# Optimization experiments

Measured on AMD Instinct MI355X. Metric: run time of the kernel, lower is better.

Reference implementation:

```python
import jax, jax.numpy as jnp
import numpy as np

B, D, M, H, L = 65536, 512, 128, 4, 2  # batch, token_dim, model_dim, heads, layers
HD = M // H
EPS = 1e-5


def _ln(x, g, b):
    m = jnp.mean(x, axis=-1, keepdims=True)
    v = jnp.mean((x - m) ** 2, axis=-1, keepdims=True)
    return (x - m) / jnp.sqrt(v + EPS) * g + b


def _mha(q, k, wqkv, bqkv, wo, bo):
    # q, k: [B, 1, M]; torch MultiheadAttention with packed in_proj ([3M, M])
    qp = jnp.einsum('bsm,nm->bsn', q, wqkv[:M]) + bqkv[:M]
    kp = jnp.einsum('bsm,nm->bsn', k, wqkv[M:2 * M]) + bqkv[M:2 * M]
    vp = jnp.einsum('bsm,nm->bsn', k, wqkv[2 * M:]) + bqkv[2 * M:]
    qh = qp.reshape(qp.shape[0], -1, H, HD).transpose(0, 2, 1, 3)
    kh = kp.reshape(kp.shape[0], -1, H, HD).transpose(0, 2, 1, 3)
    vh = vp.reshape(vp.shape[0], -1, H, HD).transpose(0, 2, 1, 3)
    scores = jnp.einsum('bhqd,bhkd->bhqk', qh, kh) / float(np.sqrt(HD))
    attn = jax.nn.softmax(scores, axis=-1)  # kv_len == 1 -> weights are 1
    o = jnp.einsum('bhqk,bhkd->bhqd', attn, vh).transpose(0, 2, 1, 3).reshape(qp.shape)
    return jnp.einsum('bsm,nm->bsn', o, wo) + bo


def _ffn(x, w1, b1, w2, b2):
    h = jax.nn.relu(jnp.einsum('bsm,nm->bsn', x, w1) + b1)
    return jnp.einsum('bsn,mn->bsm', h, w2) + b2


def _forward(transformer_tokens, eda_proj_w, eda_proj_b, imu_proj_w, imu_proj_b,
             eda_cls, imu_cls, e2i_wqkv, e2i_bqkv, e2i_wo, e2i_bo,
             i2e_wqkv, i2e_bqkv, i2e_wo, i2e_bo,
             ffn_eda_w1, ffn_eda_b1, ffn_eda_w2, ffn_eda_b2,
             ffn_imu_w1, ffn_imu_b1, ffn_imu_w2, ffn_imu_b2,
             ln_eda1_g, ln_eda1_b, ln_eda2_g, ln_eda2_b,
             ln_imu1_g, ln_imu1_b, ln_imu2_g, ln_imu2_b,
             out_w, out_b, out_ln_g, out_ln_b):
    eda_raw = transformer_tokens[:, 0, :]
    imu_raw = transformer_tokens[:, 1, :]
    eda = (jnp.einsum('bd,md->bm', eda_raw, eda_proj_w) + eda_proj_b)[:, None, :] + eda_cls
    imu = (jnp.einsum('bd,md->bm', imu_raw, imu_proj_w) + imu_proj_b)[:, None, :] + imu_cls
    for l in range(L):
        eda_attn = _mha(eda, imu, e2i_wqkv[l], e2i_bqkv[l], e2i_wo[l], e2i_bo[l])
        eda = _ln(eda + eda_attn, ln_eda1_g[l], ln_eda1_b[l])
        eda = _ln(eda + _ffn(eda, ffn_eda_w1[l], ffn_eda_b1[l], ffn_eda_w2[l], ffn_eda_b2[l]),
                  ln_eda2_g[l], ln_eda2_b[l])
        imu_attn = _mha(imu, eda, i2e_wqkv[l], i2e_bqkv[l], i2e_wo[l], i2e_bo[l])
        imu = _ln(imu + imu_attn, ln_imu1_g[l], ln_imu1_b[l])
        imu = _ln(imu + _ffn(imu, ffn_imu_w1[l], ffn_imu_b1[l], ffn_imu_w2[l], ffn_imu_b2[l]),
                  ln_imu2_g[l], ln_imu2_b[l])
    fused = jnp.concatenate([eda[:, 0, :], imu[:, 0, :]], axis=-1)  # [B, 2M]
    out = jnp.einsum('bn,mn->bm', fused, out_w) + out_b
    return jax.nn.relu(_ln(out, out_ln_g, out_ln_b))  # [B, M]


def setup_inputs() -> dict:
    key = jax.random.key(0)
    ks = jax.random.split(key, 16)
    n = lambda k, s: jax.random.normal(k, s, dtype=jnp.float32) * 0.02
    return dict(
        transformer_tokens=jax.random.normal(ks[0], (B, 2, D), dtype=jnp.float32),
        eda_proj_w=n(ks[1], (M, D)), eda_proj_b=jnp.zeros((M,), jnp.float32),
        imu_proj_w=n(ks[2], (M, D)), imu_proj_b=jnp.zeros((M,), jnp.float32),
        eda_cls=jnp.zeros((1, 1, M), jnp.float32), imu_cls=jnp.zeros((1, 1, M), jnp.float32),
        e2i_wqkv=n(ks[3], (L, 3 * M, M)), e2i_bqkv=jnp.zeros((L, 3 * M), jnp.float32),
        e2i_wo=n(ks[4], (L, M, M)), e2i_bo=jnp.zeros((L, M), jnp.float32),
        i2e_wqkv=n(ks[5], (L, 3 * M, M)), i2e_bqkv=jnp.zeros((L, 3 * M), jnp.float32),
        i2e_wo=n(ks[6], (L, M, M)), i2e_bo=jnp.zeros((L, M), jnp.float32),
        ffn_eda_w1=n(ks[7], (L, 2 * M, M)), ffn_eda_b1=jnp.zeros((L, 2 * M), jnp.float32),
        ffn_eda_w2=n(ks[8], (L, M, 2 * M)), ffn_eda_b2=jnp.zeros((L, M), jnp.float32),
        ffn_imu_w1=n(ks[9], (L, 2 * M, M)), ffn_imu_b1=jnp.zeros((L, 2 * M), jnp.float32),
        ffn_imu_w2=n(ks[10], (L, M, 2 * M)), ffn_imu_b2=jnp.zeros((L, M), jnp.float32),
        ln_eda1_g=jnp.ones((L, M), jnp.float32), ln_eda1_b=jnp.zeros((L, M), jnp.float32),
        ln_eda2_g=jnp.ones((L, M), jnp.float32), ln_eda2_b=jnp.zeros((L, M), jnp.float32),
        ln_imu1_g=jnp.ones((L, M), jnp.float32), ln_imu1_b=jnp.zeros((L, M), jnp.float32),
        ln_imu2_g=jnp.ones((L, M), jnp.float32), ln_imu2_b=jnp.zeros((L, M), jnp.float32),
        out_w=n(ks[11], (M, 2 * M)), out_b=jnp.zeros((M,), jnp.float32),
        out_ln_g=jnp.ones((M,), jnp.float32), out_ln_b=jnp.zeros((M,), jnp.float32),
    )


def reference(transformer_tokens, eda_proj_w, eda_proj_b, imu_proj_w, imu_proj_b,
              eda_cls, imu_cls, e2i_wqkv, e2i_bqkv, e2i_wo, e2i_bo,
              i2e_wqkv, i2e_bqkv, i2e_wo, i2e_bo,
              ffn_eda_w1, ffn_eda_b1, ffn_eda_w2, ffn_eda_b2,
              ffn_imu_w1, ffn_imu_b1, ffn_imu_w2, ffn_imu_b2,
              ln_eda1_g, ln_eda1_b, ln_eda2_g, ln_eda2_b,
              ln_imu1_g, ln_imu1_b, ln_imu2_g, ln_imu2_b,
              out_w, out_b, out_ln_g, out_ln_b):
    return _forward(transformer_tokens, eda_proj_w, eda_proj_b, imu_proj_w, imu_proj_b,
                    eda_cls, imu_cls, e2i_wqkv, e2i_bqkv, e2i_wo, e2i_bo,
                    i2e_wqkv, i2e_bqkv, i2e_wo, i2e_bo,
                    ffn_eda_w1, ffn_eda_b1, ffn_eda_w2, ffn_eda_b2,
                    ffn_imu_w1, ffn_imu_b1, ffn_imu_w2, ffn_imu_b2,
                    ln_eda1_g, ln_eda1_b, ln_eda2_g, ln_eda2_b,
                    ln_imu1_g, ln_imu1_b, ln_imu2_g, ln_imu2_b,
                    out_w, out_b, out_ln_g, out_ln_b)
```

## Files before the change

kernel.cpp:

```cpp
#include <hip/hip_runtime.h>
#include <hip/hip_bf16.h>


typedef __bf16 bf16x8_t __attribute__((ext_vector_type(8)));
typedef float  f32x16_t __attribute__((ext_vector_type(16)));
typedef float  f32x4_t  __attribute__((ext_vector_type(4)));

#define DEV static __device__ __forceinline__

DEV f32x16_t mfma_op(bf16x8_t a, bf16x8_t b, f32x16_t c) {
  return __builtin_amdgcn_mfma_f32_32x32x16_bf16(a, b, c, 0, 0, 0);
}

DEV bf16x8_t cvt8(const float* p) {
  f32x4_t t0 = *(const f32x4_t*)p;
  f32x4_t t1 = *(const f32x4_t*)(p + 4);
  bf16x8_t a;
  a[0] = (__bf16)t0[0]; a[1] = (__bf16)t0[1]; a[2] = (__bf16)t0[2]; a[3] = (__bf16)t0[3];
  a[4] = (__bf16)t1[0]; a[5] = (__bf16)t1[1]; a[6] = (__bf16)t1[2]; a[7] = (__bf16)t1[3];
  return a;
}

constexpr int PO_PROJ_E = 0;
constexpr int PO_PROJ_I = PO_PROJ_E + 128 * 512;
constexpr int PO_ATTN   = PO_PROJ_I + 128 * 512;
constexpr int PO_FFN1   = PO_ATTN   + 4 * 32 * 512;
constexpr int PO_FFN2   = PO_FFN1   + 4 * 64 * 512;
constexpr int PO_HEAD   = PO_FFN2   + 4 * 64 * 512;
constexpr int WS_BC_F      = 4 * 128 * 128;
constexpr int WS_PACK_BYTE = (WS_BC_F + 4 * 128) * 4;

#define PITCH_S 136
#define PITCH_H 40

__global__ __launch_bounds__(64) void prep_combine(
    const float* __restrict__ e2i_wqkv, const float* __restrict__ e2i_wo,
    const float* __restrict__ e2i_bqkv, const float* __restrict__ e2i_bo,
    const float* __restrict__ i2e_wqkv, const float* __restrict__ i2e_wo,
    const float* __restrict__ i2e_bqkv, const float* __restrict__ i2e_bo,
    float* __restrict__ wsf) {
  const int blk = blockIdx.x;
  const int d = blk >> 7, n = blk & 127, l = d & 1;
  const float* wqkv = (d < 2) ? e2i_wqkv : i2e_wqkv;
  const float* wo   = (d < 2) ? e2i_wo   : i2e_wo;
  const float* bqkv = (d < 2) ? e2i_bqkv : i2e_bqkv;
  const float* bo   = (d < 2) ? e2i_bo   : i2e_bo;
  const float* wv    = wqkv + l * 3 * 128 * 128 + 2 * 128 * 128;
  const float* worow = wo + l * 128 * 128 + n * 128;
  const float* bv    = bqkv + l * 3 * 128 + 2 * 128;
  const int lane = threadIdx.x;
  float a0 = 0.f, a1 = 0.f;
  for (int p = 0; p < 128; ++p) {
    float w = worow[p];
    a0 += w * wv[p * 128 + lane];
    a1 += w * wv[p * 128 + 64 + lane];
  }
  wsf[d * 16384 + n * 128 + lane]      = a0;
  wsf[d * 16384 + n * 128 + 64 + lane] = a1;
  float bacc = worow[lane] * bv[lane] + worow[64 + lane] * bv[64 + lane];
  for (int off = 1; off < 64; off <<= 1) bacc += __shfl_xor(bacc, off, 64);
  if (lane == 0) wsf[WS_BC_F + d * 128 + n] = bacc + bo[l * 128 + n];
}

__global__ __launch_bounds__(64) void prep_pack(
    const float* __restrict__ proj_e, const float* __restrict__ proj_i,
    const float* __restrict__ ffn_e_w1, const float* __restrict__ ffn_i_w1,
    const float* __restrict__ ffn_e_w2, const float* __restrict__ ffn_i_w2,
    const float* __restrict__ out_w, const float* __restrict__ wsf,
    __bf16* __restrict__ pack) {
  const int b = blockIdx.x, lane = threadIdx.x;
  const float* src; int K, sh, dstOff, c;
  if (b < 128)      { src = proj_e; K = 512; sh = 2; dstOff = PO_PROJ_E; c = b; }
  else if (b < 256) { src = proj_i; K = 512; sh = 2; dstOff = PO_PROJ_I; c = b - 128; }
  else if (b < 384) { int i = (b - 256) >> 5; c = (b - 256) & 31;
                      src = wsf + i * 16384; K = 128; sh = 2;
                      dstOff = PO_ATTN + i * 32 * 512; }
  else if (b < 640) { int i = (b - 384) >> 6; c = (b - 384) & 63;
                      src = ((i < 2) ? ffn_e_w1 : ffn_i_w1) + (i & 1) * 256 * 128;
                      K = 128; sh = 3; dstOff = PO_FFN1 + i * 64 * 512; }
  else if (b < 896) { int i = (b - 640) >> 6; c = (b - 640) & 63;
                      src = ((i < 2) ? ffn_e_w2 : ffn_i_w2) + (i & 1) * 128 * 256;
                      K = 256; sh = 2; dstOff = PO_FFN2 + i * 64 * 512; }
  else              { c = b - 896; src = out_w; K = 256; sh = 2; dstOff = PO_HEAD; }
  const int kt = c >> sh, nt = c & ((1 << sh) - 1);
  const int n  = nt * 32 + (lane & 31);
  const int kb = kt * 16 + (lane >> 5) * 8;
  const float* s = src + n * K + kb;
  bf16x8_t v;
#pragma unroll
  for (int j = 0; j < 8; ++j) v[j] = (__bf16)s[j];
  *(bf16x8_t*)&pack[dstOff + (c * 64 + lane) * 8] = v;
}

__global__ __launch_bounds__(64, 2) void fused_fwd(
    const float* __restrict__ tokens,
    const float* __restrict__ eda_proj_b, const float* __restrict__ eda_cls,
    const float* __restrict__ imu_proj_b, const float* __restrict__ imu_cls,
    const float* __restrict__ ffn_eda_b1, const float* __restrict__ ffn_eda_b2,
    const float* __restrict__ ffn_imu_b1, const float* __restrict__ ffn_imu_b2,
    const float* __restrict__ ln_e1g, const float* __restrict__ ln_e1b,
    const float* __restrict__ ln_e2g, const float* __restrict__ ln_e2b,
    const float* __restrict__ ln_i1g, const float* __restrict__ ln_i1b,
    const float* __restrict__ ln_i2g, const float* __restrict__ ln_i2b,
    const float* __restrict__ out_b, const float* __restrict__ out_ln_g,
    const float* __restrict__ out_ln_b,
    const float* __restrict__ bc_all,
    const __bf16* __restrict__ pack,
    float* __restrict__ out) {
  alignas(16) __shared__ __bf16 smem[2 * 32 * PITCH_S + 32 * PITCH_H];
  __bf16* Se = smem;
  __bf16* Si = smem + 32 * PITCH_S;
  __bf16* Sh = smem + 2 * 32 * PITCH_S;

  const int lane = threadIdx.x;
  const int l31 = lane & 31, lh = lane >> 5;
  const int rowbase = blockIdx.x * 32;

  auto crowf = [&](int r) { return (r & 3) + ((r >> 2) << 3) + (lh << 2); };

  auto layer_norm = [&](f32x16_t (&A)[4], const float* g, const float* bb) {
    float gv[4], bv[4];
#pragma unroll
    for (int nt = 0; nt < 4; ++nt) { gv[nt] = g[nt * 32 + l31]; bv[nt] = bb[nt * 32 + l31]; }
#pragma unroll
    for (int r = 0; r < 16; ++r) {
      float s = 0.f, s2 = 0.f;
#pragma unroll
      for (int nt = 0; nt < 4; ++nt) { float v = A[nt][r]; s += v; s2 += v * v; }
#pragma unroll
      for (int off = 1; off < 32; off <<= 1) {
        s  += __shfl_xor(s, off, 64);
        s2 += __shfl_xor(s2, off, 64);
      }
      const float mean = s * (1.f / 128.f);
      const float var  = s2 * (1.f / 128.f) - mean * mean;
      const float rs   = rsqrtf(var + 1e-5f);
#pragma unroll
      for (int nt = 0; nt < 4; ++nt)
        A[nt][r] = (A[nt][r] - mean) * rs * gv[nt] + bv[nt];
    }
  };

  auto store_state = [&](f32x16_t (&A)[4], __bf16* S) {
#pragma unroll
    for (int nt = 0; nt < 4; ++nt)
#pragma unroll
      for (int r = 0; r < 16; ++r)
        S[crowf(r) * PITCH_S + nt * 32 + l31] = (__bf16)A[nt][r];
  };

#pragma unroll 1
  for (int sel = 0; sel < 2; ++sel) {
    const float* pb = sel ? imu_proj_b : eda_proj_b;
    const float* pc = sel ? imu_cls : eda_cls;
    __bf16* Sd = sel ? Si : Se;
    const __bf16* pw = pack + (sel ? PO_PROJ_I : PO_PROJ_E);
    f32x16_t acc[4];
#pragma unroll
    for (int nt = 0; nt < 4; ++nt) {
      const float bias = pb[nt * 32 + l31] + pc[nt * 32 + l31];
#pragma unroll
      for (int r = 0; r < 16; ++r) acc[nt][r] = bias;
    }
    const float* t0 = tokens + (size_t)(rowbase + l31) * 1024 + sel * 512 + lh * 8;
#pragma unroll 1
    for (int kt = 0; kt < 32; ++kt) {
      bf16x8_t a0 = cvt8(t0 + kt * 16);
      const __bf16* pwk = pw + (kt * 4 * 64 + lane) * 8;
#pragma unroll
      for (int nt = 0; nt < 4; ++nt)
        acc[nt] = mfma_op(a0, *(const bf16x8_t*)(pwk + nt * 512), acc[nt]);
    }
    store_state(acc, Sd);
  }

#pragma unroll 1
  for (int l = 0; l < 2; ++l) {
#pragma unroll 1
    for (int mod = 0; mod < 2; ++mod) {
      const __bf16* Sx = mod ? Se : Si;
      __bf16* St = mod ? Si : Se;
      const int widx = mod * 2 + l;
      const __bf16* attn_w = pack + PO_ATTN + widx * 32 * 512;
      const __bf16* ffn1_w = pack + PO_FFN1 + widx * 64 * 512;
      const __bf16* ffn2_w = pack + PO_FFN2 + widx * 64 * 512;
      const float* bc  = bc_all + widx * 128;
      const float* b1  = (mod ? ffn_imu_b1 : ffn_eda_b1) + l * 256;
      const float* b2  = (mod ? ffn_imu_b2 : ffn_eda_b2) + l * 128;
      const float* g1  = (mod ? ln_i1g : ln_e1g) + l * 128;
      const float* bb1 = (mod ? ln_i1b : ln_e1b) + l * 128;
      const float* g2  = (mod ? ln_i2g : ln_e2g) + l * 128;
      const float* bb2 = (mod ? ln_i2b : ln_e2b) + l * 128;

      f32x16_t acc[4];
#pragma unroll
      for (int nt = 0; nt < 4; ++nt) {
        const float bv = bc[nt * 32 + l31];
#pragma unroll
        for (int r = 0; r < 16; ++r)
          acc[nt][r] = bv + (float)St[crowf(r) * PITCH_S + nt * 32 + l31];
      }
#pragma unroll 1
      for (int kt = 0; kt < 8; ++kt) {
        bf16x8_t a0 = *(const bf16x8_t*)&Sx[l31 * PITCH_S + kt * 16 + lh * 8];
        const __bf16* wk = attn_w + (kt * 4 * 64 + lane) * 8;
#pragma unroll
        for (int nt = 0; nt < 4; ++nt)
          acc[nt] = mfma_op(a0, *(const bf16x8_t*)(wk + nt * 512), acc[nt]);
      }
      layer_norm(acc, g1, bb1);
      store_state(acc, St);

      f32x16_t yacc[4];
#pragma unroll
      for (int nt = 0; nt < 4; ++nt) {
        const float bv = b2[nt * 32 + l31];
#pragma unroll
        for (int r = 0; r < 16; ++r) yacc[nt][r] = bv + acc[nt][r];
      }
#pragma unroll 1
      for (int hc = 0; hc < 8; ++hc) {
        f32x16_t h;
        {
          const float hb = b1[hc * 32 + l31];
#pragma unroll
          for (int r = 0; r < 16; ++r) h[r] = hb;
        }
        const __bf16* w1k = ffn1_w + (hc * 64 + lane) * 8;
#pragma unroll
        for (int kt = 0; kt < 8; ++kt) {
          bf16x8_t a0 = *(const bf16x8_t*)&St[l31 * PITCH_S + kt * 16 + lh * 8];
          h = mfma_op(a0, *(const bf16x8_t*)(w1k + kt * 8 * 512), h);
        }
#pragma unroll
        for (int r = 0; r < 16; ++r)
          Sh[crowf(r) * PITCH_H + l31] = (__bf16)fmaxf(h[r], 0.f);
#pragma unroll
        for (int kt2 = 0; kt2 < 2; ++kt2) {
          bf16x8_t ah = *(const bf16x8_t*)&Sh[l31 * PITCH_H + kt2 * 16 + lh * 8];
          const __bf16* w2k = ffn2_w + (((hc * 2 + kt2) * 4) * 64 + lane) * 8;
#pragma unroll
          for (int nt = 0; nt < 4; ++nt)
            yacc[nt] = mfma_op(ah, *(const bf16x8_t*)(w2k + nt * 512), yacc[nt]);
        }
      }
      layer_norm(yacc, g2, bb2);
      store_state(yacc, St);
    }
  }

  {
    f32x16_t acc[4];
#pragma unroll
    for (int nt = 0; nt < 4; ++nt) {
      const float bv = out_b[nt * 32 + l31];
#pragma unroll
      for (int r = 0; r < 16; ++r) acc[nt][r] = bv;
    }
#pragma unroll 1
    for (int kt = 0; kt < 16; ++kt) {
      const __bf16* Sa = (kt < 8) ? Se : Si;
      const int ko = (kt & 7) * 16 + lh * 8;
      bf16x8_t a0 = *(const bf16x8_t*)&Sa[l31 * PITCH_S + ko];
      const __bf16* wk = pack + PO_HEAD + (kt * 4 * 64 + lane) * 8;
#pragma unroll
      for (int nt = 0; nt < 4; ++nt)
        acc[nt] = mfma_op(a0, *(const bf16x8_t*)(wk + nt * 512), acc[nt]);
    }
    layer_norm(acc, out_ln_g, out_ln_b);
#pragma unroll
    for (int nt = 0; nt < 4; ++nt)
#pragma unroll
      for (int r = 0; r < 16; ++r)
        out[(rowbase + crowf(r)) * 128 + nt * 32 + l31] = fmaxf(acc[nt][r], 0.f);
  }
}

extern "C" void kernel_launch(void* const* d_in, const int* in_sizes, int n_in,
                              void* d_out, int out_size, void* d_ws, size_t ws_size,
                              hipStream_t stream) {
  const float* tokens     = (const float*)d_in[0];
  const float* eda_proj_w = (const float*)d_in[1];
  const float* eda_proj_b = (const float*)d_in[2];
  const float* imu_proj_w = (const float*)d_in[3];
  const float* imu_proj_b = (const float*)d_in[4];
  const float* eda_cls    = (const float*)d_in[5];
  const float* imu_cls    = (const float*)d_in[6];
  const float* e2i_wqkv   = (const float*)d_in[7];
  const float* e2i_bqkv   = (const float*)d_in[8];
  const float* e2i_wo     = (const float*)d_in[9];
  const float* e2i_bo     = (const float*)d_in[10];
  const float* i2e_wqkv   = (const float*)d_in[11];
  const float* i2e_bqkv   = (const float*)d_in[12];
  const float* i2e_wo     = (const float*)d_in[13];
  const float* i2e_bo     = (const float*)d_in[14];
  const float* ffn_eda_w1 = (const float*)d_in[15];
  const float* ffn_eda_b1 = (const float*)d_in[16];
  const float* ffn_eda_w2 = (const float*)d_in[17];
  const float* ffn_eda_b2 = (const float*)d_in[18];
  const float* ffn_imu_w1 = (const float*)d_in[19];
  const float* ffn_imu_b1 = (const float*)d_in[20];
  const float* ffn_imu_w2 = (const float*)d_in[21];
  const float* ffn_imu_b2 = (const float*)d_in[22];
  const float* ln_eda1_g  = (const float*)d_in[23];
  const float* ln_eda1_b  = (const float*)d_in[24];
  const float* ln_eda2_g  = (const float*)d_in[25];
  const float* ln_eda2_b  = (const float*)d_in[26];
  const float* ln_imu1_g  = (const float*)d_in[27];
  const float* ln_imu1_b  = (const float*)d_in[28];
  const float* ln_imu2_g  = (const float*)d_in[29];
  const float* ln_imu2_b  = (const float*)d_in[30];
  const float* out_w      = (const float*)d_in[31];
  const float* out_b      = (const float*)d_in[32];
  const float* out_ln_g   = (const float*)d_in[33];
  const float* out_ln_b   = (const float*)d_in[34];

  float*  wsf  = (float*)d_ws;
  __bf16* pack = (__bf16*)((char*)d_ws + WS_PACK_BYTE);

  prep_combine<<<dim3(512), dim3(64), 0, stream>>>(
      e2i_wqkv, e2i_wo, e2i_bqkv, e2i_bo,
      i2e_wqkv, i2e_wo, i2e_bqkv, i2e_bo, wsf);

  prep_pack<<<dim3(960), dim3(64), 0, stream>>>(
      eda_proj_w, imu_proj_w, ffn_eda_w1, ffn_imu_w1,
      ffn_eda_w2, ffn_imu_w2, out_w, wsf, pack);

  fused_fwd<<<dim3(2048), dim3(64), 0, stream>>>(
      tokens, eda_proj_b, eda_cls, imu_proj_b, imu_cls,
      ffn_eda_b1, ffn_eda_b2, ffn_imu_b1, ffn_imu_b2,
      ln_eda1_g, ln_eda1_b, ln_eda2_g, ln_eda2_b,
      ln_imu1_g, ln_imu1_b, ln_imu2_g, ln_imu2_b,
      out_b, out_ln_g, out_ln_b,
      wsf + WS_BC_F, pack, (float*)d_out);
}
```

Measured before the change: 653.1 us.

## Software-pipeline MFMA operand loads and split prep_combine reduction across four waves

The GEMM loops in the fused forward kernel (input projection, attention, FFN, head) now use explicit double buffering: the next k-step's token and weight fragments are loaded while the current MFMAs run, and in the FFN all state and weight fragments for a hidden chunk are loaded up front. This is meant to hide global and LDS load latency in a kernel that runs one wave per block. prep_combine now uses 256 threads, splitting the 128-term dot product across four waves with an LDS reduction, which shortens the serial loop. The price is higher register pressure, which could cause spills or lower occupancy.

```diff
diff --git a/kernel.cpp b/kernel.cpp
--- a/kernel.cpp
+++ b/kernel.cpp
@@ -12,9 +12,7 @@
   return __builtin_amdgcn_mfma_f32_32x32x16_bf16(a, b, c, 0, 0, 0);
 }
 
-DEV bf16x8_t cvt8(const float* p) {
-  f32x4_t t0 = *(const f32x4_t*)p;
-  f32x4_t t1 = *(const f32x4_t*)(p + 4);
+DEV bf16x8_t cvt2(f32x4_t t0, f32x4_t t1) {
   bf16x8_t a;
   a[0] = (__bf16)t0[0]; a[1] = (__bf16)t0[1]; a[2] = (__bf16)t0[2]; a[3] = (__bf16)t0[3];
   a[4] = (__bf16)t1[0]; a[5] = (__bf16)t1[1]; a[6] = (__bf16)t1[2]; a[7] = (__bf16)t1[3];
@@ -33,7 +31,7 @@
 #define PITCH_S 136
 #define PITCH_H 40
 
-__global__ __launch_bounds__(64) void prep_combine(
+__global__ __launch_bounds__(256) void prep_combine(
     const float* __restrict__ e2i_wqkv, const float* __restrict__ e2i_wo,
     const float* __restrict__ e2i_bqkv, const float* __restrict__ e2i_bo,
     const float* __restrict__ i2e_wqkv, const float* __restrict__ i2e_wo,
@@ -48,18 +46,29 @@
   const float* wv    = wqkv + l * 3 * 128 * 128 + 2 * 128 * 128;
   const float* worow = wo + l * 128 * 128 + n * 128;
   const float* bv    = bqkv + l * 3 * 128 + 2 * 128;
-  const int lane = threadIdx.x;
-  float a0 = 0.f, a1 = 0.f;
-  for (int p = 0; p < 128; ++p) {
-    float w = worow[p];
-    a0 += w * wv[p * 128 + lane];
-    a1 += w * wv[p * 128 + 64 + lane];
+  const int tid = threadIdx.x, lane = tid & 63, w = tid >> 6;
+  float a0 = 0.f, a1 = 0.f, c0 = 0.f, c1 = 0.f;
+#pragma unroll 4
+  for (int p = w * 32; p < w * 32 + 32; p += 2) {
+    float wa = worow[p], wb = worow[p + 1];
+    a0 += wa * wv[p * 128 + lane];
+    a1 += wa * wv[p * 128 + 64 + lane];
+    c0 += wb * wv[(p + 1) * 128 + lane];
+    c1 += wb * wv[(p + 1) * 128 + 64 + lane];
   }
-  wsf[d * 16384 + n * 128 + lane]      = a0;
-  wsf[d * 16384 + n * 128 + 64 + lane] = a1;
-  float bacc = worow[lane] * bv[lane] + worow[64 + lane] * bv[64 + lane];
-  for (int off = 1; off < 64; off <<= 1) bacc += __shfl_xor(bacc, off, 64);
-  if (lane == 0) wsf[WS_BC_F + d * 128 + n] = bacc + bo[l * 128 + n];
+  a0 += c0; a1 += c1;
+  __shared__ float red[4][2][64];
+  red[w][0][lane] = a0; red[w][1][lane] = a1;
+  __syncthreads();
+  if (w == 0) {
+    a0 = red[0][0][lane] + red[1][0][lane] + red[2][0][lane] + red[3][0][lane];
+    a1 = red[0][1][lane] + red[1][1][lane] + red[2][1][lane] + red[3][1][lane];
+    wsf[d * 16384 + n * 128 + lane]      = a0;
+    wsf[d * 16384 + n * 128 + 64 + lane] = a1;
+    float bacc = worow[lane] * bv[lane] + worow[64 + lane] * bv[64 + lane];
+    for (int off = 1; off < 64; off <<= 1) bacc += __shfl_xor(bacc, off, 64);
+    if (lane == 0) wsf[WS_BC_F + d * 128 + n] = bacc + bo[l * 128 + n];
+  }
 }
 
 __global__ __launch_bounds__(64) void prep_pack(
@@ -163,13 +172,43 @@
       for (int r = 0; r < 16; ++r) acc[nt][r] = bias;
     }
     const float* t0 = tokens + (size_t)(rowbase + l31) * 1024 + sel * 512 + lh * 8;
-#pragma unroll 1
-    for (int kt = 0; kt < 32; ++kt) {
-      bf16x8_t a0 = cvt8(t0 + kt * 16);
-      const __bf16* pwk = pw + (kt * 4 * 64 + lane) * 8;
-#pragma unroll
-      for (int nt = 0; nt < 4; ++nt)
-        acc[nt] = mfma_op(a0, *(const bf16x8_t*)(pwk + nt * 512), acc[nt]);
+    f32x4_t tA0 = *(const f32x4_t*)t0, tA1 = *(const f32x4_t*)(t0 + 4);
+    const __bf16* pA = pw + lane * 8;
+    bf16x8_t wA0 = *(const bf16x8_t*)(pA);
+    bf16x8_t wA1 = *(const bf16x8_t*)(pA + 512);
+    bf16x8_t wA2 = *(const bf16x8_t*)(pA + 1024);
+    bf16x8_t wA3 = *(const bf16x8_t*)(pA + 1536);
+#pragma unroll 1
+    for (int kt = 0; kt < 32; kt += 2) {
+      const float* tb = t0 + (kt + 1) * 16;
+      f32x4_t tB0 = *(const f32x4_t*)tb, tB1 = *(const f32x4_t*)(tb + 4);
+      const __bf16* pB = pw + ((kt + 1) * 4 * 64 + lane) * 8;
+      bf16x8_t wB0 = *(const bf16x8_t*)(pB);
+      bf16x8_t wB1 = *(const bf16x8_t*)(pB + 512);
+      bf16x8_t wB2 = *(const bf16x8_t*)(pB + 1024);
+      bf16x8_t wB3 = *(const bf16x8_t*)(pB + 1536);
+      {
+        bf16x8_t a = cvt2(tA0, tA1);
+        acc[0] = mfma_op(a, wA0, acc[0]);
+        acc[1] = mfma_op(a, wA1, acc[1]);
+        acc[2] = mfma_op(a, wA2, acc[2]);
+        acc[3] = mfma_op(a, wA3, acc[3]);
+      }
+      const int ka = (kt + 2 < 32) ? kt + 2 : kt;
+      const float* ta = t0 + ka * 16;
+      tA0 = *(const f32x4_t*)ta; tA1 = *(const f32x4_t*)(ta + 4);
+      pA = pw + (ka * 4 * 64 + lane) * 8;
+      wA0 = *(const bf16x8_t*)(pA);
+      wA1 = *(const bf16x8_t*)(pA + 512);
+      wA2 = *(const bf16x8_t*)(pA + 1024);
+      wA3 = *(const bf16x8_t*)(pA + 1536);
+      {
+        bf16x8_t a = cvt2(tB0, tB1);
+        acc[0] = mfma_op(a, wB0, acc[0]);
+        acc[1] = mfma_op(a, wB1, acc[1]);
+        acc[2] = mfma_op(a, wB2, acc[2]);
+        acc[3] = mfma_op(a, wB3, acc[3]);
+      }
     }
     store_state(acc, Sd);
   }
@@ -200,13 +239,37 @@
         for (int r = 0; r < 16; ++r)
           acc[nt][r] = bv + (float)St[crowf(r) * PITCH_S + nt * 32 + l31];
       }
-#pragma unroll 1
-      for (int kt = 0; kt < 8; ++kt) {
-        bf16x8_t a0 = *(const bf16x8_t*)&Sx[l31 * PITCH_S + kt * 16 + lh * 8];
-        const __bf16* wk = attn_w + (kt * 4 * 64 + lane) * 8;
-#pragma unroll
-        for (int nt = 0; nt < 4; ++nt)
-          acc[nt] = mfma_op(a0, *(const bf16x8_t*)(wk + nt * 512), acc[nt]);
+      {
+        bf16x8_t aA = *(const bf16x8_t*)&Sx[l31 * PITCH_S + lh * 8];
+        const __bf16* pA = attn_w + lane * 8;
+        bf16x8_t wA0 = *(const bf16x8_t*)(pA);
+        bf16x8_t wA1 = *(const bf16x8_t*)(pA + 512);
+        bf16x8_t wA2 = *(const bf16x8_t*)(pA + 1024);
+        bf16x8_t wA3 = *(const bf16x8_t*)(pA + 1536);
+#pragma unroll 1
+        for (int kt = 0; kt < 8; kt += 2) {
+          bf16x8_t aB = *(const bf16x8_t*)&Sx[l31 * PITCH_S + (kt + 1) * 16 + lh * 8];
+          const __bf16* pB = attn_w + ((kt + 1) * 4 * 64 + lane) * 8;
+          bf16x8_t wB0 = *(const bf16x8_t*)(pB);
+          bf16x8_t wB1 = *(const bf16x8_t*)(pB + 512);
+          bf16x8_t wB2 = *(const bf16x8_t*)(pB + 1024);
+          bf16x8_t wB3 = *(const bf16x8_t*)(pB + 1536);
+          acc[0] = mfma_op(aA, wA0, acc[0]);
+          acc[1] = mfma_op(aA, wA1, acc[1]);
+          acc[2] = mfma_op(aA, wA2, acc[2]);
+          acc[3] = mfma_op(aA, wA3, acc[3]);
+          const int ka = (kt + 2 < 8) ? kt + 2 : kt;
+          aA = *(const bf16x8_t*)&Sx[l31 * PITCH_S + ka * 16 + lh * 8];
+          pA = attn_w + (ka * 4 * 64 + lane) * 8;
+          wA0 = *(const bf16x8_t*)(pA);
+          wA1 = *(const bf16x8_t*)(pA + 512);
+          wA2 = *(const bf16x8_t*)(pA + 1024);
+          wA3 = *(const bf16x8_t*)(pA + 1536);
+          acc[0] = mfma_op(aB, wB0, acc[0]);
+          acc[1] = mfma_op(aB, wB1, acc[1]);
+          acc[2] = mfma_op(aB, wB2, acc[2]);
+          acc[3] = mfma_op(aB, wB3, acc[3]);
+        }
       }
       layer_norm(acc, g1, bb1);
       store_state(acc, St);
@@ -220,29 +283,55 @@
       }
 #pragma unroll 1
       for (int hc = 0; hc < 8; ++hc) {
+        bf16x8_t s0 = *(const bf16x8_t*)&St[l31 * PITCH_S + 0 * 16 + lh * 8];
+        bf16x8_t s1 = *(const bf16x8_t*)&St[l31 * PITCH_S + 1 * 16 + lh * 8];
+        bf16x8_t s2 = *(const bf16x8_t*)&St[l31 * PITCH_S + 2 * 16 + lh * 8];
+        bf16x8_t s3 = *(const bf16x8_t*)&St[l31 * PITCH_S + 3 * 16 + lh * 8];
+        bf16x8_t s4 = *(const bf16x8_t*)&St[l31 * PITCH_S + 4 * 16 + lh * 8];
+        bf16x8_t s5 = *(const bf16x8_t*)&St[l31 * PITCH_S + 5 * 16 + lh * 8];
+        bf16x8_t s6 = *(const bf16x8_t*)&St[l31 * PITCH_S + 6 * 16 + lh * 8];
+        bf16x8_t s7 = *(const bf16x8_t*)&St[l31 * PITCH_S + 7 * 16 + lh * 8];
+        const __bf16* w1b = ffn1_w + (hc * 64 + lane) * 8;
+        bf16x8_t u0 = *(const bf16x8_t*)(w1b + 0 * 8 * 512);
+        bf16x8_t u1 = *(const bf16x8_t*)(w1b + 1 * 8 * 512);
+        bf16x8_t u2 = *(const bf16x8_t*)(w1b + 2 * 8 * 512);
+        bf16x8_t u3 = *(const bf16x8_t*)(w1b + 3 * 8 * 512);
+        bf16x8_t u4 = *(const bf16x8_t*)(w1b + 4 * 8 * 512);
+        bf16x8_t u5 = *(const bf16x8_t*)(w1b + 5 * 8 * 512);
+        bf16x8_t u6 = *(const bf16x8_t*)(w1b + 6 * 8 * 512);
+        bf16x8_t u7 = *(const bf16x8_t*)(w1b + 7 * 8 * 512);
+        const __bf16* w2b = ffn2_w + (hc * 8 * 64 + lane) * 8;
+        bf16x8_t v0 = *(const bf16x8_t*)(w2b + 0 * 512);
+        bf16x8_t v1 = *(const bf16x8_t*)(w2b + 1 * 512);
+        bf16x8_t v2 = *(const bf16x8_t*)(w2b + 2 * 512);
+        bf16x8_t v3 = *(const bf16x8_t*)(w2b + 3 * 512);
+        bf16x8_t v4 = *(const bf16x8_t*)(w2b + 4 * 512);
+        bf16x8_t v5 = *(const bf16x8_t*)(w2b + 5 * 512);
+        bf16x8_t v6 = *(const bf16x8_t*)(w2b + 6 * 512);
+        bf16x8_t v7 = *(const bf16x8_t*)(w2b + 7 * 512);
         f32x16_t h;
         {
           const float hb = b1[hc * 32 + l31];
 #pragma unroll
           for (int r = 0; r < 16; ++r) h[r] = hb;
         }
-        const __bf16* w1k = ffn1_w + (hc * 64 + lane) * 8;
-#pragma unroll
-        for (int kt = 0; kt < 8; ++kt) {
-          bf16x8_t a0 = *(const bf16x8_t*)&St[l31 * PITCH_S + kt * 16 + lh * 8];
-          h = mfma_op(a0, *(const bf16x8_t*)(w1k + kt * 8 * 512), h);
-        }
+        h = mfma_op(s0, u0, h); h = mfma_op(s1, u1, h);
+        h = mfma_op(s2, u2, h); h = mfma_op(s3, u3, h);
+        h = mfma_op(s4, u4, h); h = mfma_op(s5, u5, h);
+        h = mfma_op(s6, u6, h); h = mfma_op(s7, u7, h);
 #pragma unroll
         for (int r = 0; r < 16; ++r)
           Sh[crowf(r) * PITCH_H + l31] = (__bf16)fmaxf(h[r], 0.f);
-#pragma unroll
-        for (int kt2 = 0; kt2 < 2; ++kt2) {
-          bf16x8_t ah = *(const bf16x8_t*)&Sh[l31 * PITCH_H + kt2 * 16 + lh * 8];
-          const __bf16* w2k = ffn2_w + (((hc * 2 + kt2) * 4) * 64 + lane) * 8;
-#pragma unroll
-          for (int nt = 0; nt < 4; ++nt)
-            yacc[nt] = mfma_op(ah, *(const bf16x8_t*)(w2k + nt * 512), yacc[nt]);
-        }
+        bf16x8_t ah0 = *(const bf16x8_t*)&Sh[l31 * PITCH_H + lh * 8];
+        bf16x8_t ah1 = *(const bf16x8_t*)&Sh[l31 * PITCH_H + 16 + lh * 8];
+        yacc[0] = mfma_op(ah0, v0, yacc[0]);
+        yacc[1] = mfma_op(ah0, v1, yacc[1]);
+        yacc[2] = mfma_op(ah0, v2, yacc[2]);
+        yacc[3] = mfma_op(ah0, v3, yacc[3]);
+        yacc[0] = mfma_op(ah1, v4, yacc[0]);
+        yacc[1] = mfma_op(ah1, v5, yacc[1]);
+        yacc[2] = mfma_op(ah1, v6, yacc[2]);
+        yacc[3] = mfma_op(ah1, v7, yacc[3]);
       }
       layer_norm(yacc, g2, bb2);
       store_state(yacc, St);
@@ -257,15 +346,38 @@
 #pragma unroll
       for (int r = 0; r < 16; ++r) acc[nt][r] = bv;
     }
-#pragma unroll 1
-    for (int kt = 0; kt < 16; ++kt) {
-      const __bf16* Sa = (kt < 8) ? Se : Si;
-      const int ko = (kt & 7) * 16 + lh * 8;
-      bf16x8_t a0 = *(const bf16x8_t*)&Sa[l31 * PITCH_S + ko];
-      const __bf16* wk = pack + PO_HEAD + (kt * 4 * 64 + lane) * 8;
-#pragma unroll
-      for (int nt = 0; nt < 4; ++nt)
-        acc[nt] = mfma_op(a0, *(const bf16x8_t*)(wk + nt * 512), acc[nt]);
+    const __bf16* hw = pack + PO_HEAD;
+    bf16x8_t aA = *(const bf16x8_t*)&Se[l31 * PITCH_S + lh * 8];
+    const __bf16* pA = hw + lane * 8;
+    bf16x8_t wA0 = *(const bf16x8_t*)(pA);
+    bf16x8_t wA1 = *(const bf16x8_t*)(pA + 512);
+    bf16x8_t wA2 = *(const bf16x8_t*)(pA + 1024);
+    bf16x8_t wA3 = *(const bf16x8_t*)(pA + 1536);
+#pragma unroll 1
+    for (int kt = 0; kt < 16; kt += 2) {
+      const __bf16* SaB = (kt + 1 < 8) ? Se : Si;
+      bf16x8_t aB = *(const bf16x8_t*)&SaB[l31 * PITCH_S + ((kt + 1) & 7) * 16 + lh * 8];
+      const __bf16* pB = hw + ((kt + 1) * 4 * 64 + lane) * 8;
+      bf16x8_t wB0 = *(const bf16x8_t*)(pB);
+      bf16x8_t wB1 = *(const bf16x8_t*)(pB + 512);
+      bf16x8_t wB2 = *(const bf16x8_t*)(pB + 1024);
+      bf16x8_t wB3 = *(const bf16x8_t*)(pB + 1536);
+      acc[0] = mfma_op(aA, wA0, acc[0]);
+      acc[1] = mfma_op(aA, wA1, acc[1]);
+      acc[2] = mfma_op(aA, wA2, acc[2]);
+      acc[3] = mfma_op(aA, wA3, acc[3]);
+      const int ka = (kt + 2 < 16) ? kt + 2 : kt;
+      const __bf16* SaA = (ka < 8) ? Se : Si;
+      aA = *(const bf16x8_t*)&SaA[l31 * PITCH_S + (ka & 7) * 16 + lh * 8];
+      pA = hw + (ka * 4 * 64 + lane) * 8;
+      wA0 = *(const bf16x8_t*)(pA);
+      wA1 = *(const bf16x8_t*)(pA + 512);
+      wA2 = *(const bf16x8_t*)(pA + 1024);
+      wA3 = *(const bf16x8_t*)(pA + 1536);
+      acc[0] = mfma_op(aB, wB0, acc[0]);
+      acc[1] = mfma_op(aB, wB1, acc[1]);
+      acc[2] = mfma_op(aB, wB2, acc[2]);
+      acc[3] = mfma_op(aB, wB3, acc[3]);
     }
     layer_norm(acc, out_ln_g, out_ln_b);
 #pragma unroll
@@ -318,7 +430,7 @@
   float*  wsf  = (float*)d_ws;
   __bf16* pack = (__bf16*)((char*)d_ws + WS_PACK_BYTE);
 
-  prep_combine<<<dim3(512), dim3(64), 0, stream>>>(
+  prep_combine<<<dim3(512), dim3(256), 0, stream>>>(
       e2i_wqkv, e2i_wo, e2i_bqkv, e2i_bo,
       i2e_wqkv, i2e_wo, i2e_bqkv, i2e_bo, wsf);
 
```

New measurement: 662.9 us. About the same (+1.5%).
